# Kernel tuning notes

Hardware: AMD Instinct MI355X
Metric: run time of the kernel (lower is better)

## Reference

```python
import jax, jax.numpy as jnp
import numpy as np

B, S = 8, 512          # batch, seq_len
D, F = 1024, 2048      # d_model, head hidden dim
H = 16                 # num_tasks (= num heads)
V = 3000               # selfies vocab
O = 1                  # head output size
INIT = 0.02


def setup_inputs() -> dict:
    key = jax.random.key(0)
    ks = jax.random.split(key, 12)
    return {
        "selfies": jax.random.randint(ks[0], (B, S), 0, V),
        "tasks": jax.random.randint(ks[1], (B, S), 0, H + 1),  # 0 -> invalid (-1)
        "values": jax.random.normal(ks[2], (B, S), jnp.float32),
        "property_mask": jax.random.randint(ks[3], (B, S), 0, 2).astype(bool),
        # shared_base params (embed + FFN -> [B,S,D])
        "emb_selfies": jax.random.normal(ks[4], (V, D), jnp.float32) * INIT,
        "emb_tasks": jax.random.normal(ks[5], (H + 1, D), jnp.float32) * INIT,
        "val_vec": jax.random.normal(ks[6], (D,), jnp.float32) * INIT,
        "Ws": jax.random.normal(ks[7], (D, D), jnp.float32) * INIT,
        "bs": jnp.zeros((D,), jnp.float32),
        # stacked per-head MLP params: Linear(D,F) -> GELU -> Linear(F,O)
        "W1": jax.random.normal(ks[8], (H, D, F), jnp.float32) * INIT,
        "b1": jnp.zeros((H, F), jnp.float32),
        "W2": jax.random.normal(ks[9], (H, F, O), jnp.float32) * INIT,
        "b2": jnp.zeros((H, O), jnp.float32),
    }


def reference(selfies, tasks, values, property_mask,
              emb_selfies, emb_tasks, val_vec, Ws, bs, W1, b1, W2, b2):
    # ---- shared_base: embed + masked token features + FFN -> [B,S,D] ----
    h = (emb_selfies[selfies] + emb_tasks[tasks] + values[..., None] * val_vec)
    h = h * property_mask[..., None].astype(h.dtype)
    shared = jax.nn.gelu(h @ Ws + bs)                      # [B,S,D]

    # ---- routing: task token -> head index, 0 means invalid (-1) ----
    head_idx = jnp.where(tasks > 0, (tasks - 1) % H, -1)   # [B,S]

    # ---- each active head runs its MLP over the FULL shared_output ----
    hid = jax.nn.gelu(jnp.einsum('bsd,hdf->bshf', shared, W1) + b1)  # [B,S,H,F]
    heads_out = jnp.einsum('bshf,hfo->bsho', hid, W2) + b2           # [B,S,H,O]

    # ---- scatter/select per token by head index; invalid -> zeros ----
    idx = jnp.clip(head_idx, 0)
    out = jnp.take_along_axis(heads_out, idx[..., None, None], axis=2)[:, :, 0, :]
    return jnp.where(head_idx[..., None] >= 0, out, jnp.zeros_like(out))
```

## Files before the change

### kernel.cpp

```cpp
#include <hip/hip_runtime.h>
#include <hip/hip_bf16.h>

#define TOK 4096
#define DD  1024
#define FF  2048
#define NH  16

typedef short bf16x8 __attribute__((ext_vector_type(8)));
typedef float f32x4  __attribute__((ext_vector_type(4)));

__device__ __forceinline__ float gelu_f(float x) {
  float u = 0.7978845608028654f * (x + 0.044715f * x * x * x);
  float e = __expf(2.0f * u);
  return 0.5f * x * (2.0f - 2.0f / (e + 1.0f));
}

__device__ __forceinline__ unsigned short f2bf(float f) {
  union { float f; unsigned u; } v; v.f = f;
  unsigned r = v.u + 0x7FFF + ((v.u >> 16) & 1);
  return (unsigned short)(r >> 16);
}
__device__ __forceinline__ unsigned pack2(float a, float b) {
  return (unsigned)f2bf(a) | ((unsigned)f2bf(b) << 16);
}

__device__ __forceinline__ void load_lds16(const void* g, void* l) {
  __builtin_amdgcn_global_load_lds(
      (const __attribute__((address_space(1))) void*)g,
      (__attribute__((address_space(3))) void*)l, 16, 0, 0);
}

__global__ __launch_bounds__(256) void route_kernel(
    const int* __restrict__ tasks, const float* __restrict__ b2,
    int* __restrict__ counts, int* __restrict__ lists, float* __restrict__ out) {
  int t = blockIdx.x * 256 + threadIdx.x;
  if (t >= TOK) return;
  int task = tasks[t];
  if (task > 0) {
    int h = (task - 1) & (NH - 1);
    int pos = atomicAdd(&counts[h], 1);
    lists[h * TOK + pos] = t;
    out[t] = b2[h];
  } else {
    out[t] = 0.0f;
  }
}

__global__ __launch_bounds__(256) void prep_x(
    const int* __restrict__ selfies, const int* __restrict__ tasks,
    const float* __restrict__ values, const int* __restrict__ pmask,
    const float* __restrict__ emb_s, const float* __restrict__ emb_t,
    const float* __restrict__ val_vec, unsigned short* __restrict__ Xb) {
  int gid = blockIdx.x * 256 + threadIdx.x;
  int kc = (gid & 127) * 8;
  int t  = gid >> 7;
  int sid = selfies[t], tsk = tasks[t];
  float v = values[t];
  float msk = pmask[t] ? 1.0f : 0.0f;
  const float* ps = emb_s + (size_t)sid * DD + kc;
  const float* pt = emb_t + (size_t)tsk * DD + kc;
  const float* pv = val_vec + kc;
  float r[8];
#pragma unroll
  for (int j = 0; j < 8; j += 4) {
    float4 a = *(const float4*)(ps + j);
    float4 b = *(const float4*)(pt + j);
    float4 c = *(const float4*)(pv + j);
    r[j + 0] = (a.x + b.x + v * c.x) * msk;
    r[j + 1] = (a.y + b.y + v * c.y) * msk;
    r[j + 2] = (a.z + b.z + v * c.z) * msk;
    r[j + 3] = (a.w + b.w + v * c.w) * msk;
  }
  uint4 o;
  o.x = pack2(r[0], r[1]); o.y = pack2(r[2], r[3]);
  o.z = pack2(r[4], r[5]); o.w = pack2(r[6], r[7]);
  *(uint4*)(Xb + (size_t)gid * 8) = o;
}

__global__ __launch_bounds__(256) void prep_w(
    const float* __restrict__ Ws, const float* __restrict__ W1,
    unsigned short* __restrict__ Wsp, unsigned short* __restrict__ W1p) {
  int cid = blockIdx.x * 256 + threadIdx.x;
  const float* src;
  unsigned short* dst;
  int stride;
  if (cid < 16 * 128 * 32 * 64) {
    int lane = cid & 63, kc2 = (cid >> 6) & 31, nt = (cid >> 11) & 127, h = cid >> 18;
    src = W1 + ((size_t)h * DD + kc2 * 32 + (lane >> 4) * 8) * FF + nt * 16 + (lane & 15);
    dst = W1p + (size_t)cid * 8;
    stride = FF;
  } else {
    int cid2 = cid - 16 * 128 * 32 * 64;
    int lane = cid2 & 63, kc2 = (cid2 >> 6) & 31, nt = cid2 >> 11;
    src = Ws + ((size_t)kc2 * 32 + (lane >> 4) * 8) * DD + nt * 16 + (lane & 15);
    dst = Wsp + (size_t)cid2 * 8;
    stride = DD;
  }
  float r[8];
#pragma unroll
  for (int j = 0; j < 8; ++j) r[j] = src[(size_t)j * stride];
  uint4 o;
  o.x = pack2(r[0], r[1]); o.y = pack2(r[2], r[3]);
  o.z = pack2(r[4], r[5]); o.w = pack2(r[6], r[7]);
  *(uint4*)dst = o;
}

__global__ __launch_bounds__(256) void gemm1_mfma(
    const unsigned short* __restrict__ Xb, const unsigned short* __restrict__ Wsp,
    const float* __restrict__ bs, unsigned short* __restrict__ shared_bf) {
  __shared__ __align__(16) unsigned short As[2][2 * 4 * 64 * 8];
  __shared__ __align__(16) unsigned short Bs[2][2 * 8 * 64 * 8];

  const int tid = threadIdx.x;
  const int lane = tid & 63, w = tid >> 6;
  const int m0 = blockIdx.x * 64;
  const int n0 = blockIdx.y * 128;
  const int q = lane >> 4, c = lane & 15;

  const unsigned short* aSrc = Xb + (size_t)(m0 + w * 16 + c) * DD + q * 8;
  const unsigned short* bBase = Wsp + ((size_t)(blockIdx.y * 8 + w * 2)) * 32 * 512 + lane * 8;
  f32x4 acc[4][2] = {};

  auto stage = [&](int buf, int k0) {
    load_lds16(aSrc + k0,      As[buf] + (size_t)(0 * 256 + w * 64 + lane) * 8);
    load_lds16(aSrc + k0 + 32, As[buf] + (size_t)(1 * 256 + w * 64 + lane) * 8);
    const unsigned short* bk = bBase + k0 * 16;
#pragma unroll
    for (int i = 0; i < 4; ++i) {
      int kk = i >> 1, t = i & 1;
      load_lds16(bk + (size_t)t * 16384 + kk * 512,
                 Bs[buf] + (size_t)(kk * 8 + w * 2 + t) * 512 + lane * 8);
    }
  };
  auto compute = [&](int buf) {
#pragma unroll
    for (int kk = 0; kk < 2; ++kk) {
      bf16x8 a[4], b[2];
#pragma unroll
      for (int mt = 0; mt < 4; ++mt)
        a[mt] = *(const bf16x8*)(As[buf] + (size_t)((kk * 4 + mt) * 64 + lane) * 8);
#pragma unroll
      for (int t = 0; t < 2; ++t)
        b[t] = *(const bf16x8*)(Bs[buf] + (size_t)((kk * 8 + w * 2 + t) * 64 + lane) * 8);
#pragma unroll
      for (int mt = 0; mt < 4; ++mt)
#pragma unroll
        for (int t = 0; t < 2; ++t)
          acc[mt][t] = __builtin_amdgcn_mfma_f32_16x16x32_bf16(a[mt], b[t], acc[mt][t], 0, 0, 0);
    }
  };

  stage(0, 0);
  __syncthreads();
  int cur = 0;
  for (int k0 = 64; k0 < DD; k0 += 64) {
    stage(cur ^ 1, k0);
    compute(cur);
    __syncthreads();
    cur ^= 1;
  }
  compute(cur);

  float bsv[2];
#pragma unroll
  for (int t = 0; t < 2; ++t) bsv[t] = bs[n0 + w * 32 + t * 16 + c];
#pragma unroll
  for (int mt = 0; mt < 4; ++mt)
#pragma unroll
    for (int t = 0; t < 2; ++t)
#pragma unroll
      for (int r = 0; r < 4; ++r) {
        int row = m0 + mt * 16 + q * 4 + r;
        int col = n0 + w * 32 + t * 16 + c;
        shared_bf[(size_t)row * DD + col] = f2bf(gelu_f(acc[mt][t][r] + bsv[t]));
      }
}

__global__ __launch_bounds__(256) void gemm2_mfma(
    const unsigned short* __restrict__ shared_bf, const unsigned short* __restrict__ W1p,
    const float* __restrict__ b1, const float* __restrict__ W2,
    const int* __restrict__ counts, const int* __restrict__ lists,
    float* __restrict__ out) {
  const int h = blockIdx.z;
  const int nt_h = counts[h];
  const int m0 = blockIdx.x * 64;
  if (m0 >= nt_h) return;
  const int fc = blockIdx.y;

  __shared__ __align__(16) unsigned short As[2][2 * 4 * 64 * 8];
  __shared__ __align__(16) unsigned short Bs[2][2 * 8 * 64 * 8];
  __shared__ int   stok[64];
  __shared__ float red[4][68];

  const int tid = threadIdx.x;
  const int lane = tid & 63, w = tid >> 6;
  const int q = lane >> 4, c = lane & 15;

  if (tid < 64) {
    int i = m0 + tid;
    stok[tid] = (i < nt_h) ? lists[h * TOK + i] : -1;
  }
  __syncthreads();

  int tokr = stok[w * 16 + c];
  if (tokr < 0) tokr = 0;
  const unsigned short* aSrc = shared_bf + (size_t)tokr * DD + q * 8;

  const unsigned short* bBase =
      W1p + ((size_t)h * 128 + fc * 8 + w * 2) * 32 * 512 + lane * 8;

  f32x4 acc[4][2] = {};

  auto stage = [&](int buf, int k0) {
    load_lds16(aSrc + k0,      As[buf] + (size_t)(0 * 256 + w * 64 + lane) * 8);
    load_lds16(aSrc + k0 + 32, As[buf] + (size_t)(1 * 256 + w * 64 + lane) * 8);
    const unsigned short* bk = bBase + k0 * 16;
#pragma unroll
    for (int i = 0; i < 4; ++i) {
      int kk = i >> 1, t = i & 1;
      load_lds16(bk + (size_t)t * 16384 + kk * 512,
                 Bs[buf] + (size_t)(kk * 8 + w * 2 + t) * 512 + lane * 8);
    }
  };
  auto compute = [&](int buf) {
#pragma unroll
    for (int kk = 0; kk < 2; ++kk) {
      bf16x8 a[4], b[2];
#pragma unroll
      for (int mt = 0; mt < 4; ++mt)
        a[mt] = *(const bf16x8*)(As[buf] + (size_t)((kk * 4 + mt) * 64 + lane) * 8);
#pragma unroll
      for (int t = 0; t < 2; ++t)
        b[t] = *(const bf16x8*)(Bs[buf] + (size_t)((kk * 8 + w * 2 + t) * 64 + lane) * 8);
#pragma unroll
      for (int mt = 0; mt < 4; ++mt)
#pragma unroll
        for (int t = 0; t < 2; ++t)
          acc[mt][t] = __builtin_amdgcn_mfma_f32_16x16x32_bf16(a[mt], b[t], acc[mt][t], 0, 0, 0);
    }
  };

  stage(0, 0);
  __syncthreads();
  int cur = 0;
  for (int k0 = 64; k0 < DD; k0 += 64) {
    stage(cur ^ 1, k0);
    compute(cur);
    __syncthreads();
    cur ^= 1;
  }
  compute(cur);

  const float* b1h = b1 + (size_t)h * FF + fc * 128 + w * 32;
  const float* w2h = W2 + (size_t)h * FF + fc * 128 + w * 32;
  float b1v[2], w2v[2];
#pragma unroll
  for (int t = 0; t < 2; ++t) { b1v[t] = b1h[t * 16 + c]; w2v[t] = w2h[t * 16 + c]; }

#pragma unroll
  for (int mt = 0; mt < 4; ++mt)
#pragma unroll
    for (int r = 0; r < 4; ++r) {
      float s = 0.0f;
#pragma unroll
      for (int t = 0; t < 2; ++t)
        s += gelu_f(acc[mt][t][r] + b1v[t]) * w2v[t];
      s += __shfl_xor(s, 1);
      s += __shfl_xor(s, 2);
      s += __shfl_xor(s, 4);
      s += __shfl_xor(s, 8);
      if (c == 0) red[w][mt * 16 + q * 4 + r] = s;
    }
  __syncthreads();

  if (tid < 64) {
    int t = stok[tid];
    if (t >= 0) {
      float s = red[0][tid] + red[1][tid] + red[2][tid] + red[3][tid];
      atomicAdd(&out[t], s);
    }
  }
}

extern "C" void kernel_launch(void* const* d_in, const int* in_sizes, int n_in,
                              void* d_out, int out_size, void* d_ws, size_t ws_size,
                              hipStream_t stream) {
  const int*   selfies = (const int*)d_in[0];
  const int*   tasks   = (const int*)d_in[1];
  const float* values  = (const float*)d_in[2];
  const int*   pmask   = (const int*)d_in[3];
  const float* emb_s   = (const float*)d_in[4];
  const float* emb_t   = (const float*)d_in[5];
  const float* val_vec = (const float*)d_in[6];
  const float* Ws      = (const float*)d_in[7];
  const float* bs      = (const float*)d_in[8];
  const float* W1      = (const float*)d_in[9];
  const float* b1      = (const float*)d_in[10];
  const float* W2      = (const float*)d_in[11];
  const float* b2      = (const float*)d_in[12];
  float* out = (float*)d_out;

  char* ws = (char*)d_ws;
  unsigned short* Xb        = (unsigned short*)ws;
  unsigned short* shared_bf = (unsigned short*)(ws + (8u << 20));
  unsigned short* Wsp       = (unsigned short*)(ws + (16u << 20));
  unsigned short* W1p       = (unsigned short*)(ws + (18u << 20));
  int* counts = (int*)(ws + (82u << 20));
  int* lists  = (int*)(ws + (82u << 20) + 256);

  hipMemsetAsync(counts, 0, NH * sizeof(int), stream);
  route_kernel<<<TOK / 256, 256, 0, stream>>>(tasks, b2, counts, lists, out);
  prep_x<<<TOK * 128 / 256, 256, 0, stream>>>(selfies, tasks, values, pmask,
                                              emb_s, emb_t, val_vec, Xb);
  prep_w<<<(16 * 128 * 32 * 64 + 64 * 32 * 64) / 256, 256, 0, stream>>>(Ws, W1, Wsp, W1p);
  gemm1_mfma<<<dim3(TOK / 64, DD / 128), 256, 0, stream>>>(Xb, Wsp, bs, shared_bf);
  gemm2_mfma<<<dim3(8, FF / 128, NH), 256, 0, stream>>>(shared_bf, W1p, b1, W2,
                                                        counts, lists, out);
}
```

Baseline: 358.8 us.

## Tile weight prep through LDS, deepen GEMM prefetch, remap gemm2 blocks per XCD

prep_w now loads 64x64 fp32 tiles with coalesced float4 reads, converts them to bf16 in LDS, and writes the MFMA-packed layout from there. The old version issued strided scalar reads, and this 134MB fp32 W1 read likely dominates the runtime. Both GEMMs switch to a prefetch-two-ahead schedule with manual vmcnt waits and raw barriers, and hoist the bias and W2 loads before the main loop. gemm2 uses a 1D grid whose block ids are mapped so each XCD handles whole heads, which should improve L2 reuse of W1p. The hand-written waitcnt counts are fragile if the compiler changes the number of outstanding loads.

```diff
diff --git a/kernel.cpp b/kernel.cpp
--- a/kernel.cpp
+++ b/kernel.cpp
@@ -77,32 +77,60 @@
   *(uint4*)(Xb + (size_t)gid * 8) = o;
 }
 
+#define W1_TILES (16 * 16 * 32)
+#define WS_TILES (16 * 16)
+
 __global__ __launch_bounds__(256) void prep_w(
     const float* __restrict__ Ws, const float* __restrict__ W1,
     unsigned short* __restrict__ Wsp, unsigned short* __restrict__ W1p) {
-  int cid = blockIdx.x * 256 + threadIdx.x;
-  const float* src;
-  unsigned short* dst;
-  int stride;
-  if (cid < 16 * 128 * 32 * 64) {
-    int lane = cid & 63, kc2 = (cid >> 6) & 31, nt = (cid >> 11) & 127, h = cid >> 18;
-    src = W1 + ((size_t)h * DD + kc2 * 32 + (lane >> 4) * 8) * FF + nt * 16 + (lane & 15);
-    dst = W1p + (size_t)cid * 8;
+  __shared__ unsigned short T[64][70];
+  int bid = blockIdx.x;
+  const float* src; unsigned short* dstBase; int stride, nt0, kc0;
+  if (bid < W1_TILES) {
+    int fb = bid & 31, kb = (bid >> 5) & 15, h = bid >> 9;
+    src = W1 + ((size_t)h * DD + kb * 64) * FF + fb * 64;
     stride = FF;
+    nt0 = h * 128 + fb * 4;
+    kc0 = kb * 2;
+    dstBase = W1p;
   } else {
-    int cid2 = cid - 16 * 128 * 32 * 64;
-    int lane = cid2 & 63, kc2 = (cid2 >> 6) & 31, nt = cid2 >> 11;
-    src = Ws + ((size_t)kc2 * 32 + (lane >> 4) * 8) * DD + nt * 16 + (lane & 15);
-    dst = Wsp + (size_t)cid2 * 8;
+    int b2 = bid - W1_TILES;
+    int fb = b2 & 15, kb = b2 >> 4;
+    src = Ws + (size_t)(kb * 64) * DD + fb * 64;
     stride = DD;
-  }
-  float r[8];
-#pragma unroll
-  for (int j = 0; j < 8; ++j) r[j] = src[(size_t)j * stride];
-  uint4 o;
-  o.x = pack2(r[0], r[1]); o.y = pack2(r[2], r[3]);
-  o.z = pack2(r[4], r[5]); o.w = pack2(r[6], r[7]);
-  *(uint4*)dst = o;
+    nt0 = fb * 4;
+    kc0 = kb * 2;
+    dstBase = Wsp;
+  }
+  const int tid = threadIdx.x;
+  {
+    int r = tid >> 2, cq = (tid & 3) * 16;
+    const float* p = src + (size_t)r * stride + cq;
+#pragma unroll
+    for (int i = 0; i < 4; ++i) {
+      float4 v = *(const float4*)(p + i * 4);
+      *(unsigned*)&T[r][cq + i * 4 + 0] = pack2(v.x, v.y);
+      *(unsigned*)&T[r][cq + i * 4 + 2] = pack2(v.z, v.w);
+    }
+  }
+  __syncthreads();
+#pragma unroll
+  for (int cc = 0; cc < 2; ++cc) {
+    int idx = tid + cc * 256;
+    int lane2 = idx & 63, kcl = (idx >> 6) & 1, ntl = idx >> 7;
+    int n_local = ntl * 16 + (lane2 & 15);
+    int r0 = kcl * 32 + (lane2 >> 4) * 8;
+    unsigned short e[8];
+#pragma unroll
+    for (int j = 0; j < 8; ++j) e[j] = T[r0 + j][n_local];
+    uint4 o;
+    o.x = (unsigned)e[0] | ((unsigned)e[1] << 16);
+    o.y = (unsigned)e[2] | ((unsigned)e[3] << 16);
+    o.z = (unsigned)e[4] | ((unsigned)e[5] << 16);
+    o.w = (unsigned)e[6] | ((unsigned)e[7] << 16);
+    size_t chunk = ((size_t)(nt0 + ntl) * 32 + (kc0 + kcl)) * 64 + lane2;
+    *(uint4*)(dstBase + chunk * 8) = o;
+  }
 }
 
 __global__ __launch_bounds__(256) void gemm1_mfma(
@@ -121,6 +149,11 @@
   const unsigned short* bBase = Wsp + ((size_t)(blockIdx.y * 8 + w * 2)) * 32 * 512 + lane * 8;
   f32x4 acc[4][2] = {};
 
+  float bsv[2];
+  bsv[0] = bs[n0 + w * 32 + c];
+  bsv[1] = bs[n0 + w * 32 + 16 + c];
+  asm volatile("" :: "v"(bsv[0]), "v"(bsv[1]));
+
   auto stage = [&](int buf, int k0) {
     load_lds16(aSrc + k0,      As[buf] + (size_t)(0 * 256 + w * 64 + lane) * 8);
     load_lds16(aSrc + k0 + 32, As[buf] + (size_t)(1 * 256 + w * 64 + lane) * 8);
@@ -151,19 +184,24 @@
   };
 
   stage(0, 0);
-  __syncthreads();
+  stage(1, 64);
+  asm volatile("s_waitcnt vmcnt(6)" ::: "memory");
+  __builtin_amdgcn_s_barrier();
   int cur = 0;
-  for (int k0 = 64; k0 < DD; k0 += 64) {
-    stage(cur ^ 1, k0);
+  for (int i = 0; i < 14; ++i) {
     compute(cur);
-    __syncthreads();
+    asm volatile("" ::: "memory");
+    __builtin_amdgcn_s_barrier();
+    stage(cur, (i + 2) * 64);
+    asm volatile("s_waitcnt vmcnt(6)" ::: "memory");
+    __builtin_amdgcn_s_barrier();
     cur ^= 1;
   }
   compute(cur);
-
-  float bsv[2];
-#pragma unroll
-  for (int t = 0; t < 2; ++t) bsv[t] = bs[n0 + w * 32 + t * 16 + c];
+  asm volatile("s_waitcnt vmcnt(0)" ::: "memory");
+  __builtin_amdgcn_s_barrier();
+  compute(cur ^ 1);
+
 #pragma unroll
   for (int mt = 0; mt < 4; ++mt)
 #pragma unroll
@@ -181,11 +219,14 @@
     const float* __restrict__ b1, const float* __restrict__ W2,
     const int* __restrict__ counts, const int* __restrict__ lists,
     float* __restrict__ out) {
-  const int h = blockIdx.z;
+  const int id = blockIdx.x;
+  const int xcd = id & 7, local_ = id >> 3;
+  const int h = xcd + 8 * (local_ >> 7);
+  const int rest = local_ & 127;
+  const int fc = rest & 15;
+  const int m0 = (rest >> 4) * 64;
   const int nt_h = counts[h];
-  const int m0 = blockIdx.x * 64;
   if (m0 >= nt_h) return;
-  const int fc = blockIdx.y;
 
   __shared__ __align__(16) unsigned short As[2][2 * 4 * 64 * 8];
   __shared__ __align__(16) unsigned short Bs[2][2 * 8 * 64 * 8];
@@ -205,11 +246,17 @@
   int tokr = stok[w * 16 + c];
   if (tokr < 0) tokr = 0;
   const unsigned short* aSrc = shared_bf + (size_t)tokr * DD + q * 8;
-
   const unsigned short* bBase =
       W1p + ((size_t)h * 128 + fc * 8 + w * 2) * 32 * 512 + lane * 8;
 
   f32x4 acc[4][2] = {};
+
+  const float* b1h = b1 + (size_t)h * FF + fc * 128 + w * 32;
+  const float* w2h = W2 + (size_t)h * FF + fc * 128 + w * 32;
+  float b1v[2], w2v[2];
+  b1v[0] = b1h[c];      b1v[1] = b1h[16 + c];
+  w2v[0] = w2h[c];      w2v[1] = w2h[16 + c];
+  asm volatile("" :: "v"(b1v[0]), "v"(b1v[1]), "v"(w2v[0]), "v"(w2v[1]));
 
   auto stage = [&](int buf, int k0) {
     load_lds16(aSrc + k0,      As[buf] + (size_t)(0 * 256 + w * 64 + lane) * 8);
@@ -241,21 +288,23 @@
   };
 
   stage(0, 0);
-  __syncthreads();
+  stage(1, 64);
+  asm volatile("s_waitcnt vmcnt(6)" ::: "memory");
+  __builtin_amdgcn_s_barrier();
   int cur = 0;
-  for (int k0 = 64; k0 < DD; k0 += 64) {
-    stage(cur ^ 1, k0);
+  for (int i = 0; i < 14; ++i) {
     compute(cur);
-    __syncthreads();
+    asm volatile("" ::: "memory");
+    __builtin_amdgcn_s_barrier();
+    stage(cur, (i + 2) * 64);
+    asm volatile("s_waitcnt vmcnt(6)" ::: "memory");
+    __builtin_amdgcn_s_barrier();
     cur ^= 1;
   }
   compute(cur);
-
-  const float* b1h = b1 + (size_t)h * FF + fc * 128 + w * 32;
-  const float* w2h = W2 + (size_t)h * FF + fc * 128 + w * 32;
-  float b1v[2], w2v[2];
-#pragma unroll
-  for (int t = 0; t < 2; ++t) { b1v[t] = b1h[t * 16 + c]; w2v[t] = w2h[t * 16 + c]; }
+  asm volatile("s_waitcnt vmcnt(0)" ::: "memory");
+  __builtin_amdgcn_s_barrier();
+  compute(cur ^ 1);
 
 #pragma unroll
   for (int mt = 0; mt < 4; ++mt)
@@ -312,8 +361,8 @@
   route_kernel<<<TOK / 256, 256, 0, stream>>>(tasks, b2, counts, lists, out);
   prep_x<<<TOK * 128 / 256, 256, 0, stream>>>(selfies, tasks, values, pmask,
                                               emb_s, emb_t, val_vec, Xb);
-  prep_w<<<(16 * 128 * 32 * 64 + 64 * 32 * 64) / 256, 256, 0, stream>>>(Ws, W1, Wsp, W1p);
+  prep_w<<<W1_TILES + WS_TILES, 256, 0, stream>>>(Ws, W1, Wsp, W1p);
   gemm1_mfma<<<dim3(TOK / 64, DD / 128), 256, 0, stream>>>(Xb, Wsp, bs, shared_bf);
-  gemm2_mfma<<<dim3(8, FF / 128, NH), 256, 0, stream>>>(shared_bf, W1p, b1, W2,
-                                                        counts, lists, out);
-}
+  gemm2_mfma<<<2048, 256, 0, stream>>>(shared_bf, W1p, b1, W2,
+                                       counts, lists, out);
+}
```

After: 320.2 us. -10.8%, faster.
